# Kernel tuning notes

Hardware: AMD Instinct MI355X
Metric: run time of the kernel (lower is better)

The kernel has to match this reference:

```python
import jax, jax.numpy as jnp
import numpy as np

B, C, N = 8, 512, 2048

def setup_inputs() -> dict:
    key = jax.random.key(0)
    ks = jax.random.split(key, 7)
    s = 1.0 / np.sqrt(C)
    return {
        "x": jax.random.normal(ks[0], (B, C, N), dtype=jnp.float32),
        "wq": jax.random.normal(ks[1], (C, C), dtype=jnp.float32) * s,
        "bq": jax.random.normal(ks[2], (C,), dtype=jnp.float32) * s,
        "wk": jax.random.normal(ks[3], (C, C), dtype=jnp.float32) * s,
        "bk": jax.random.normal(ks[4], (C,), dtype=jnp.float32) * s,
        "wv": jax.random.normal(ks[5], (C, C), dtype=jnp.float32) * s,
        "bv": jax.random.normal(ks[6], (C,), dtype=jnp.float32) * s,
    }

def reference(x, wq, bq, wk, bk, wv, bv):
    # Conv1d with kernel=1 == pointwise channel matmul: [B,C,N] -> [B,C,N]
    q = jnp.einsum('oc,bcn->bon', wq, x) + bq[None, :, None]
    k = jnp.einsum('oc,bcn->bon', wk, x) + bk[None, :, None]
    v = jnp.einsum('oc,bcn->bon', wv, x) + bv[None, :, None]
    # scores[b,i,j] = sum_c q[b,c,i] * k[b,c,j]; softmax over j (no scaling, as in source)
    scores = jnp.einsum('bci,bcj->bij', q, k)
    attn = jax.nn.softmax(scores, axis=-1)  # [B,N,N]
    # out[b,c,i] = sum_j v[b,c,j] * attn[b,i,j]
    out = jnp.einsum('bcj,bij->bci', v, attn)
    return out + x
```

## Files before the change

kernel.cpp:

```cpp
#include <hip/hip_runtime.h>
#include <hip/hip_bf16.h>

typedef _Float16 half_t;
typedef _Float16 f16x8 __attribute__((ext_vector_type(8)));
typedef float f32x4 __attribute__((ext_vector_type(4)));

#define AS1 __attribute__((address_space(1)))
#define AS3 __attribute__((address_space(3)))

constexpr int CB = 512;
constexpr int NB = 2048;
constexpr int BB = 8;

__device__ inline f32x4 mfma16(f16x8 a, f16x8 b, f32x4 c) {
  return __builtin_amdgcn_mfma_f32_16x16x32_f16(a, b, c, 0, 0, 0);
}

__global__ void convert_w(const float* __restrict__ wv, half_t* __restrict__ wvh) {
  int i = blockIdx.x * 256 + threadIdx.x;
  if (i < CB * CB) wvh[i] = (half_t)wv[i];
}

__global__ __launch_bounds__(256) void compute_G_part(const float* __restrict__ wq,
                                                      const float* __restrict__ wk,
                                                      float* __restrict__ Gp) {
  __shared__ float aq[64][68];
  __shared__ float ak[64][68];
  const int c0 = blockIdx.y * 64, d0 = blockIdx.x * 64, o0 = blockIdx.z * 64;
  const int t = threadIdx.x;
  {
    const int r = t >> 2, cbase = (t & 3) * 16;
    const float* q = wq + (size_t)(o0 + r) * CB + c0 + cbase;
    const float* k = wk + (size_t)(o0 + r) * CB + d0 + cbase;
#pragma unroll
    for (int q4 = 0; q4 < 4; q4++) {
      *(float4*)&aq[r][cbase + q4 * 4] = *(const float4*)(q + q4 * 4);
      *(float4*)&ak[r][cbase + q4 * 4] = *(const float4*)(k + q4 * 4);
    }
  }
  __syncthreads();
  const int tc = t & 15, td = t >> 4;
  float acc[4][4] = {};
#pragma unroll 8
  for (int o = 0; o < 64; o++) {
    float4 a4 = *(const float4*)&aq[o][tc * 4];
    float4 b4 = *(const float4*)&ak[o][td * 4];
    float av[4] = {a4.x, a4.y, a4.z, a4.w};
    float bv[4] = {b4.x, b4.y, b4.z, b4.w};
#pragma unroll
    for (int i = 0; i < 4; i++)
#pragma unroll
      for (int j = 0; j < 4; j++)
        acc[i][j] += av[i] * bv[j];
  }
  float* gz = Gp + (size_t)blockIdx.z * CB * CB;
#pragma unroll
  for (int i = 0; i < 4; i++) {
    int c = c0 + tc * 4 + i;
#pragma unroll
    for (int j = 0; j < 4; j++)
      gz[(size_t)c * CB + d0 + td * 4 + j] = acc[i][j];
  }
}

__global__ void reduce_G(const float* __restrict__ Gp, half_t* __restrict__ Gh) {
  int i = blockIdx.x * 256 + threadIdx.x;
  if (i >= CB * CB) return;
  float s = 0.0f;
#pragma unroll
  for (int z = 0; z < 8; z++) s += Gp[(size_t)z * CB * CB + i];
  Gh[i] = (half_t)s;
}

__global__ void compute_u(const float* __restrict__ wk, const float* __restrict__ bq,
                          float* __restrict__ u) {
  int d = blockIdx.x * 256 + threadIdx.x;
  if (d >= CB) return;
  float s = 0.0f;
  for (int o = 0; o < CB; o++) s += bq[o] * wk[(size_t)o * CB + d];
  u[d] = s;
}

__global__ __launch_bounds__(256) void compute_ubias(const half_t* __restrict__ xh,
                                                     const float* __restrict__ u,
                                                     float* __restrict__ ub) {
  __shared__ float us[CB];
  for (int i = threadIdx.x; i < CB; i += 256) us[i] = u[i];
  __syncthreads();
  int row = blockIdx.x * 4 + (threadIdx.x >> 6);
  int lane = threadIdx.x & 63;
  f16x8 vh = *(const f16x8*)(xh + (size_t)row * CB + lane * 8);
  float s = 0.0f;
#pragma unroll
  for (int i = 0; i < 8; i++) s += us[lane * 8 + i] * (float)vh[i];
#pragma unroll
  for (int off = 32; off; off >>= 1) s += __shfl_xor(s, off);
  if (lane == 0) ub[row] = s;
}

__global__ void transpose_x(const float* __restrict__ x, half_t* __restrict__ oh) {
  __shared__ float tile[32][33];
  int b = blockIdx.z, c0 = blockIdx.y * 32, n0 = blockIdx.x * 32;
  int tx = threadIdx.x, ty = threadIdx.y;
  const float* xb = x + (size_t)b * CB * NB;
#pragma unroll
  for (int r = 0; r < 4; r++)
    tile[ty + 8 * r][tx] = xb[(size_t)(c0 + ty + 8 * r) * NB + n0 + tx];
  __syncthreads();
  size_t base = (size_t)b * NB * CB;
#pragma unroll
  for (int r = 0; r < 4; r++)
    oh[base + (size_t)(n0 + ty + 8 * r) * CB + c0 + tx] = (half_t)tile[tx][ty + 8 * r];
}

template <int BIAS, int EPI, int BSPLIT>
__global__ __launch_bounds__(256) void gemm_nt(
    const half_t* __restrict__ A, int lda, long sA,
    const half_t* __restrict__ Bh, const half_t* __restrict__ Bl, int ldb, long sB,
    void* __restrict__ D, int ldd, long sD,
    const float* __restrict__ bias, long sBias,
    const float* __restrict__ R, int ldr, long sR,
    int K) {
  constexpr int PL = 2 + BSPLIT;
  constexpr int TSZ = 128 * 32;
  __shared__ alignas(16) half_t sm[2 * PL * TSZ];

  const int t = threadIdx.x;
  const int z = blockIdx.z;
  const half_t* Ab  = A  + (size_t)z * sA + (size_t)(blockIdx.y * 128) * lda;
  const half_t* Bbh = Bh + (size_t)z * sB + (size_t)(blockIdx.x * 128) * ldb;
  const half_t* Bbl = BSPLIT ? Bl + (size_t)z * sB + (size_t)(blockIdx.x * 128) * ldb : nullptr;
  const int wid = t >> 6, l15 = t & 15, hi = (t >> 4) & 3;
  const int wr = wid >> 1, wc = wid & 1;
  const int lineA = t >> 2, eoff = (t & 3) * 8;

  f32x4 acc[4][4] = {};

  auto stage = [&](int buf, int kt) {
    half_t* base = sm + buf * (PL * TSZ);
#pragma unroll
    for (int p = 0; p < 2; p++) {
      size_t goA = (size_t)(p * 64 + lineA) * lda + kt * 32 + eoff;
      size_t goB = (size_t)(p * 64 + lineA) * ldb + kt * 32 + eoff;
      int lo = p * 2048 + t * 8;
      __builtin_amdgcn_global_load_lds((const AS1 void*)(Ab + goA),  (AS3 void*)(base + lo), 16, 0, 0);
      __builtin_amdgcn_global_load_lds((const AS1 void*)(Bbh + goB), (AS3 void*)(base + TSZ + lo), 16, 0, 0);
      if (BSPLIT)
        __builtin_amdgcn_global_load_lds((const AS1 void*)(Bbl + goB), (AS3 void*)(base + 2 * TSZ + lo), 16, 0, 0);
    }
  };

  const int nt = K >> 5;
  stage(0, 0);
  __syncthreads();
  int cur = 0;
  for (int kt = 0; kt < nt; kt++) {
    if (kt + 1 < nt) stage(cur ^ 1, kt + 1);
    const half_t* bb = sm + cur * (PL * TSZ);
    f16x8 af[4], bfh[4], bfl[4];
#pragma unroll
    for (int f = 0; f < 4; f++) {
      int ao = (wr * 64 + f * 16 + l15) * 32 + hi * 8;
      int bo = (wc * 64 + f * 16 + l15) * 32 + hi * 8;
      af[f]  = *(const f16x8*)(bb + ao);
      bfh[f] = *(const f16x8*)(bb + TSZ + bo);
      if (BSPLIT) bfl[f] = *(const f16x8*)(bb + 2 * TSZ + bo);
    }
#pragma unroll
    for (int pass = 0; pass < 1 + BSPLIT; pass++) {
#pragma unroll
      for (int fm = 0; fm < 4; fm++)
#pragma unroll
        for (int fn = 0; fn < 4; fn++)
          acc[fm][fn] = mfma16(af[fm], (pass == 1) ? bfl[fn] : bfh[fn], acc[fm][fn]);
    }
    __syncthreads();
    cur ^= 1;
  }

  const int row0 = blockIdx.y * 128 + wr * 64;
  const int col0 = blockIdx.x * 128 + wc * 64;
#pragma unroll
  for (int fm = 0; fm < 4; fm++) {
    int rowb = row0 + fm * 16 + hi * 4;
#pragma unroll
    for (int fn = 0; fn < 4; fn++) {
      int col = col0 + fn * 16 + l15;
      float bc = (BIAS == 1) ? bias[(size_t)z * sBias + col] : 0.0f;
#pragma unroll
      for (int r = 0; r < 4; r++) {
        float val = acc[fm][fn][r] + bc;
        if (BIAS == 2) val += bias[(size_t)z * sBias + rowb + r];
        size_t di = (size_t)(rowb + r) * ldd + col;
        if (EPI == 0) {
          ((float*)D)[(size_t)z * sD + di] = val;
        } else if (EPI == 1) {
          ((half_t*)D)[(size_t)z * sD + di] = (half_t)val;
        } else if (EPI == 2) {
          val += R[(size_t)z * sR + (size_t)(rowb + r) * ldr + col];
          ((float*)D)[(size_t)z * sD + di] = val;
        } else {
          float sv = fminf(fmaxf(val * 256.0f, -32767.0f), 32767.0f);
          ((short*)D)[(size_t)z * sD + di] = (short)__float2int_rn(sv);
        }
      }
    }
  }
}

struct alignas(16) H8 { half_t h[8]; };
struct alignas(16) S8 { short s[8]; };

__global__ __launch_bounds__(256) void softmax_rows(const short* __restrict__ S,
                                                    half_t* __restrict__ P) {
  const short* row = S + (size_t)blockIdx.x * NB;
  int t = threadIdx.x;
  S8 r8 = *reinterpret_cast<const S8*>(row + t * 8);
  float vals[8];
#pragma unroll
  for (int i = 0; i < 8; i++) vals[i] = (float)r8.s[i] * 0.00390625f;
  float m = vals[0];
#pragma unroll
  for (int i = 1; i < 8; i++) m = fmaxf(m, vals[i]);
#pragma unroll
  for (int off = 32; off; off >>= 1) m = fmaxf(m, __shfl_xor(m, off));
  __shared__ float redm[4], reds[4];
  if ((t & 63) == 0) redm[t >> 6] = m;
  __syncthreads();
  m = fmaxf(fmaxf(redm[0], redm[1]), fmaxf(redm[2], redm[3]));
  float e[8], s = 0.0f;
#pragma unroll
  for (int i = 0; i < 8; i++) { e[i] = __expf(vals[i] - m); s += e[i]; }
#pragma unroll
  for (int off = 32; off; off >>= 1) s += __shfl_xor(s, off);
  if ((t & 63) == 0) reds[t >> 6] = s;
  __syncthreads();
  s = reds[0] + reds[1] + reds[2] + reds[3];
  float inv = 1.0f / s;
  H8 ob;
#pragma unroll
  for (int i = 0; i < 8; i++) ob.h[i] = (half_t)(e[i] * inv);
  *reinterpret_cast<H8*>(P + (size_t)blockIdx.x * NB + t * 8) = ob;
}

extern "C" void kernel_launch(void* const* d_in, const int* in_sizes, int n_in,
                              void* d_out, int out_size, void* d_ws, size_t ws_size,
                              hipStream_t stream) {
  const float* x  = (const float*)d_in[0];
  const float* wq = (const float*)d_in[1];
  const float* bq = (const float*)d_in[2];
  const float* wk = (const float*)d_in[3];
  const float* wv = (const float*)d_in[5];
  const float* bv = (const float*)d_in[6];
  float* out = (float*)d_out;

  const size_t MB = 1u << 20;
  if (ws_size < 180 * MB) return;

  char* ws = (char*)d_ws;
  half_t* xh   = (half_t*)(ws + 0);
  half_t* YTh  = (half_t*)(ws + 16 * MB);
  half_t* v    = (half_t*)(ws + 32 * MB);
  short*  Ss   = (short*)(ws + 48 * MB);
  float*  Gp   = (float*)(ws + 48 * MB);
  half_t* Pd   = (half_t*)(ws + 112 * MB);
  half_t* Gh   = (half_t*)(ws + 176 * MB);
  half_t* wvh  = (half_t*)(ws + 176 * MB + 512 * 1024);
  float*  u    = (float*)(ws + 177 * MB);
  float*  ub   = (float*)(ws + 177 * MB + 256 * 1024);

  convert_w<<<1024, 256, 0, stream>>>(wv, wvh);
  compute_G_part<<<dim3(8, 8, 8), 256, 0, stream>>>(wq, wk, Gp);
  reduce_G<<<1024, 256, 0, stream>>>(Gp, Gh);
  compute_u<<<2, 256, 0, stream>>>(wk, bq, u);
  transpose_x<<<dim3(64, 16, 8), dim3(32, 8), 0, stream>>>(x, xh);
  compute_ubias<<<BB * NB / 4, 256, 0, stream>>>(xh, u, ub);

  gemm_nt<0, 1, 0><<<dim3(4, 16, 8), 256, 0, stream>>>(
      xh, CB, (long)NB * CB, Gh, nullptr, CB, 0,
      YTh, CB, (long)NB * CB, nullptr, 0, nullptr, 0, 0, CB);

  gemm_nt<2, 1, 0><<<dim3(16, 4, 8), 256, 0, stream>>>(
      wvh, CB, 0, xh, nullptr, CB, (long)NB * CB,
      v, NB, (long)CB * NB, bv, 0, nullptr, 0, 0, CB);

  gemm_nt<1, 4, 0><<<dim3(16, 16, 8), 256, 0, stream>>>(
      xh, CB, (long)NB * CB,
      YTh, nullptr, CB, (long)NB * CB,
      Ss, NB, (long)NB * NB, ub, NB, nullptr, 0, 0, CB);

  softmax_rows<<<BB * NB, 256, 0, stream>>>(Ss, Pd);

  gemm_nt<0, 2, 0><<<dim3(16, 4, 8), 256, 0, stream>>>(
      v, NB, (long)CB * NB,
      Pd, nullptr, NB, (long)NB * NB,
      out, NB, (long)CB * NB, nullptr, 0,
      x, NB, (long)CB * NB, NB);
}
```

Baseline: 207.4 us.

## Add dedicated 128x64-tile PV GEMM with fp16 residual copy of x

Replaces the generic 128x128 gemm_nt for the final attention-times-V product with a specialized gemm_pv kernel. It uses 128x64 output tiles, which doubles the number of blocks for the K=2048 reduction and should improve load balance across CUs. The transpose kernel now also writes an untransposed fp16 copy of x, and the epilogue adds the residual from that copy instead of the fp32 input. This halves residual read bytes in the epilogue but costs an extra 16 MB write up front and rounds the residual to fp16. The unused R residual parameters are removed from gemm_nt.

```diff
diff --git a/kernel.cpp b/kernel.cpp
--- a/kernel.cpp
+++ b/kernel.cpp
@@ -98,14 +98,19 @@
   if (lane == 0) ub[row] = s;
 }
 
-__global__ void transpose_x(const float* __restrict__ x, half_t* __restrict__ oh) {
+__global__ void transpose_x(const float* __restrict__ x, half_t* __restrict__ oh,
+                            half_t* __restrict__ xn) {
   __shared__ float tile[32][33];
   int b = blockIdx.z, c0 = blockIdx.y * 32, n0 = blockIdx.x * 32;
   int tx = threadIdx.x, ty = threadIdx.y;
   const float* xb = x + (size_t)b * CB * NB;
-#pragma unroll
-  for (int r = 0; r < 4; r++)
-    tile[ty + 8 * r][tx] = xb[(size_t)(c0 + ty + 8 * r) * NB + n0 + tx];
+  half_t* xnb = xn + (size_t)b * CB * NB;
+#pragma unroll
+  for (int r = 0; r < 4; r++) {
+    float v = xb[(size_t)(c0 + ty + 8 * r) * NB + n0 + tx];
+    tile[ty + 8 * r][tx] = v;
+    xnb[(size_t)(c0 + ty + 8 * r) * NB + n0 + tx] = (half_t)v;
+  }
   __syncthreads();
   size_t base = (size_t)b * NB * CB;
 #pragma unroll
@@ -119,7 +124,6 @@
     const half_t* __restrict__ Bh, const half_t* __restrict__ Bl, int ldb, long sB,
     void* __restrict__ D, int ldd, long sD,
     const float* __restrict__ bias, long sBias,
-    const float* __restrict__ R, int ldr, long sR,
     int K) {
   constexpr int PL = 2 + BSPLIT;
   constexpr int TSZ = 128 * 32;
@@ -196,14 +200,81 @@
           ((float*)D)[(size_t)z * sD + di] = val;
         } else if (EPI == 1) {
           ((half_t*)D)[(size_t)z * sD + di] = (half_t)val;
-        } else if (EPI == 2) {
-          val += R[(size_t)z * sR + (size_t)(rowb + r) * ldr + col];
-          ((float*)D)[(size_t)z * sD + di] = val;
         } else {
           float sv = fminf(fmaxf(val * 256.0f, -32767.0f), 32767.0f);
           ((short*)D)[(size_t)z * sD + di] = (short)__float2int_rn(sv);
         }
       }
+    }
+  }
+}
+
+__global__ __launch_bounds__(256) void gemm_pv(
+    const half_t* __restrict__ V, const half_t* __restrict__ P,
+    const half_t* __restrict__ Rn, float* __restrict__ D) {
+  constexpr int ATSZ = 128 * 32;
+  constexpr int BTSZ = 64 * 32;
+  constexpr int BUF = ATSZ + BTSZ;
+  __shared__ alignas(16) half_t sm[2 * BUF];
+
+  const int t = threadIdx.x, z = blockIdx.z;
+  const half_t* Ab = V + (size_t)z * CB * NB + (size_t)(blockIdx.y * 128) * NB;
+  const half_t* Bb = P + (size_t)z * NB * NB + (size_t)(blockIdx.x * 64) * NB;
+  const int wid = t >> 6, l15 = t & 15, hi = (t >> 4) & 3;
+  const int wr = wid >> 1, wc = wid & 1;
+  const int lineA = t >> 2, eoff = (t & 3) * 8;
+
+  f32x4 acc[4][2] = {};
+
+  auto stage = [&](int buf, int kt) {
+    half_t* base = sm + buf * BUF;
+#pragma unroll
+    for (int p = 0; p < 2; p++) {
+      size_t go = (size_t)(p * 64 + lineA) * NB + kt * 32 + eoff;
+      __builtin_amdgcn_global_load_lds((const AS1 void*)(Ab + go),
+                                       (AS3 void*)(base + p * 2048 + t * 8), 16, 0, 0);
+    }
+    size_t gb = (size_t)lineA * NB + kt * 32 + eoff;
+    __builtin_amdgcn_global_load_lds((const AS1 void*)(Bb + gb),
+                                     (AS3 void*)(base + ATSZ + t * 8), 16, 0, 0);
+  };
+
+  stage(0, 0);
+  __syncthreads();
+  int cur = 0;
+  for (int kt = 0; kt < 64; kt++) {
+    if (kt + 1 < 64) stage(cur ^ 1, kt + 1);
+    const half_t* bb = sm + cur * BUF;
+    f16x8 af[4], bf[2];
+#pragma unroll
+    for (int f = 0; f < 4; f++)
+      af[f] = *(const f16x8*)(bb + (wr * 64 + f * 16 + l15) * 32 + hi * 8);
+#pragma unroll
+    for (int f = 0; f < 2; f++)
+      bf[f] = *(const f16x8*)(bb + ATSZ + (wc * 32 + f * 16 + l15) * 32 + hi * 8);
+#pragma unroll
+    for (int fm = 0; fm < 4; fm++)
+#pragma unroll
+      for (int fn = 0; fn < 2; fn++)
+        acc[fm][fn] = mfma16(af[fm], bf[fn], acc[fm][fn]);
+    __syncthreads();
+    cur ^= 1;
+  }
+
+  const int row0 = blockIdx.y * 128 + wr * 64;
+  const int col0 = blockIdx.x * 64 + wc * 32;
+  float* Dz = D + (size_t)z * CB * NB;
+  const half_t* Rz = Rn + (size_t)z * CB * NB;
+#pragma unroll
+  for (int fm = 0; fm < 4; fm++) {
+    int rowb = row0 + fm * 16 + hi * 4;
+#pragma unroll
+    for (int fn = 0; fn < 2; fn++) {
+      int col = col0 + fn * 16 + l15;
+#pragma unroll
+      for (int r = 0; r < 4; r++)
+        Dz[(size_t)(rowb + r) * NB + col] =
+            acc[fm][fn][r] + (float)Rz[(size_t)(rowb + r) * NB + col];
     }
   }
 }
@@ -255,7 +326,7 @@
   float* out = (float*)d_out;
 
   const size_t MB = 1u << 20;
-  if (ws_size < 180 * MB) return;
+  if (ws_size < 196 * MB) return;
 
   char* ws = (char*)d_ws;
   half_t* xh   = (half_t*)(ws + 0);
@@ -264,36 +335,33 @@
   short*  Ss   = (short*)(ws + 48 * MB);
   float*  Gp   = (float*)(ws + 48 * MB);
   half_t* Pd   = (half_t*)(ws + 112 * MB);
-  half_t* Gh   = (half_t*)(ws + 176 * MB);
-  half_t* wvh  = (half_t*)(ws + 176 * MB + 512 * 1024);
-  float*  u    = (float*)(ws + 177 * MB);
-  float*  ub   = (float*)(ws + 177 * MB + 256 * 1024);
+  half_t* xn   = (half_t*)(ws + 176 * MB);
+  half_t* Gh   = (half_t*)(ws + 192 * MB);
+  half_t* wvh  = (half_t*)(ws + 192 * MB + 512 * 1024);
+  float*  u    = (float*)(ws + 193 * MB);
+  float*  ub   = (float*)(ws + 193 * MB + 256 * 1024);
 
   convert_w<<<1024, 256, 0, stream>>>(wv, wvh);
   compute_G_part<<<dim3(8, 8, 8), 256, 0, stream>>>(wq, wk, Gp);
   reduce_G<<<1024, 256, 0, stream>>>(Gp, Gh);
   compute_u<<<2, 256, 0, stream>>>(wk, bq, u);
-  transpose_x<<<dim3(64, 16, 8), dim3(32, 8), 0, stream>>>(x, xh);
+  transpose_x<<<dim3(64, 16, 8), dim3(32, 8), 0, stream>>>(x, xh, xn);
   compute_ubias<<<BB * NB / 4, 256, 0, stream>>>(xh, u, ub);
 
   gemm_nt<0, 1, 0><<<dim3(4, 16, 8), 256, 0, stream>>>(
       xh, CB, (long)NB * CB, Gh, nullptr, CB, 0,
-      YTh, CB, (long)NB * CB, nullptr, 0, nullptr, 0, 0, CB);
+      YTh, CB, (long)NB * CB, nullptr, 0, CB);
 
   gemm_nt<2, 1, 0><<<dim3(16, 4, 8), 256, 0, stream>>>(
       wvh, CB, 0, xh, nullptr, CB, (long)NB * CB,
-      v, NB, (long)CB * NB, bv, 0, nullptr, 0, 0, CB);
+      v, NB, (long)CB * NB, bv, 0, CB);
 
   gemm_nt<1, 4, 0><<<dim3(16, 16, 8), 256, 0, stream>>>(
       xh, CB, (long)NB * CB,
       YTh, nullptr, CB, (long)NB * CB,
-      Ss, NB, (long)NB * NB, ub, NB, nullptr, 0, 0, CB);
+      Ss, NB, (long)NB * NB, ub, NB, CB);
 
   softmax_rows<<<BB * NB, 256, 0, stream>>>(Ss, Pd);
 
-  gemm_nt<0, 2, 0><<<dim3(16, 4, 8), 256, 0, stream>>>(
-      v, NB, (long)CB * NB,
-      Pd, nullptr, NB, (long)NB * NB,
-      out, NB, (long)CB * NB, nullptr, 0,
-      x, NB, (long)CB * NB, NB);
-}
+  gemm_pv<<<dim3(32, 4, 8), 256, 0, stream>>>(v, Pd, xn, out);
+}
```

Measured after the change: 222.5 us. 1.07x slower.
